# Performance work log

Measured on AMD Instinct MI355X. Metric: run time of the kernel, lower is better.

Reference implementation:

```python
import jax, jax.numpy as jnp
import numpy as np

B, LQ, LK, D = 16, 1024, 4096, 256
SQRT_SCALE_INV = 0.25          # D ** -0.25, so scale = 1/sqrt(D)
HALF_BW = 128 // 2             # stripe_bandwdith // 2
NEG_INF = float('-inf')


def setup_inputs() -> dict:
    key = jax.random.key(0)
    k1, k2, k3, k4 = jax.random.split(key, 4)
    query = jax.random.normal(k1, (B, LQ, D), jnp.float32)
    key_t = jax.random.normal(k2, (B, LK, D), jnp.float32)
    value = jax.random.normal(k3, (B, LK, D), jnp.float32)
    # key lengths in [LK//2, LK]; masked_fill in torch requires max == LK
    key_lengths = jax.random.randint(k4, (B,), LK // 2, LK + 1).astype(jnp.int32)
    key_lengths = key_lengths.at[0].set(LK)
    query_lengths = jnp.full((B,), LQ, dtype=jnp.int32)  # full so no all-masked rows
    mask = jnp.arange(LK)[None, :] < key_lengths[:, None]  # [B, LK] bool, True = valid
    return {"query": query, "key": key_t, "value": value, "mask": mask,
            "query_lengths": query_lengths, "key_lengths": key_lengths}


def _stripe_mask(query_lengths, key_lengths, Lq, Lk):
    # band around line y = x * (key_len / query_len), per sample
    gx = jnp.arange(Lq, dtype=jnp.float32)[None, :, None]   # [1,Lq,1]
    gy = jnp.arange(Lk, dtype=jnp.float32)[None, None, :]   # [1,1,Lk]
    slope = (key_lengths.astype(jnp.float32) /
             query_lengths.astype(jnp.float32))[:, None, None]  # [B,1,1]
    center = gx * slope
    return (gy >= center - HALF_BW) & (gy <= center + HALF_BW)  # [B,Lq,Lk] bool


def reference(query, key, value, mask, query_lengths, key_lengths):
    # scores = (q * s) @ (k * s)^T  ==  (q @ k^T) * s^2
    scores = jnp.einsum('bqd,bkd->bqk', query, key) * (SQRT_SCALE_INV * SQRT_SCALE_INV)
    stripe = _stripe_mask(query_lengths, key_lengths, query.shape[1], key.shape[1])
    full_mask = mask[:, None, :] & stripe                    # padding AND stripe
    scores = jnp.where(full_mask, scores.astype(jnp.float32), NEG_INF)
    weight = jax.nn.softmax(scores, axis=-1).astype(query.dtype)
    # module applies no dropout (p=0) and returns (attn_weight, value)
    return (weight, value)
```

## Files before the change

kernel.cpp:

```cpp
#include <hip/hip_runtime.h>
#include <math.h>

constexpr int B_  = 16;
constexpr int LQ_ = 1024;
constexpr int LK_ = 4096;
constexpr int D_  = 256;
constexpr float HALF_BW_F = 64.0f;
constexpr float SCALE = 0.0625f;

typedef float fx4 __attribute__((ext_vector_type(4)));

constexpr int NB_PAD = 168;
constexpr int ROWS_PER_BLK = 16;
constexpr int NBLK = (B_ * LQ_) / ROWS_PER_BLK;
constexpr int NXCD = 8;
constexpr int BLK_PER_XCD = NBLK / NXCD;

template <int CTRL>
__device__ __forceinline__ float dpp_add(float v) {
    int x = __builtin_amdgcn_update_dpp(0, __float_as_int(v), CTRL, 0xF, 0xF, true);
    return v + __int_as_float(x);
}

__device__ __forceinline__ float grp16_max(float v) {
    #pragma unroll
    for (int off = 8; off > 0; off >>= 1)
        v = fmaxf(v, __shfl_xor(v, off, 64));
    return v;
}
__device__ __forceinline__ float grp16_sum(float v) {
    #pragma unroll
    for (int off = 8; off > 0; off >>= 1)
        v += __shfl_xor(v, off, 64);
    return v;
}

__global__ __launch_bounds__(256, 4) void stripe_attn_kernel(
    const float* __restrict__ Q, const float* __restrict__ K,
    const float* __restrict__ V,
    const int* __restrict__ qlen, const int* __restrict__ klen,
    float* __restrict__ Wout, float* __restrict__ Vout)
{
    const int rb   = (blockIdx.x & (NXCD - 1)) * BLK_PER_XCD + (blockIdx.x >> 3);
    const int tid  = threadIdx.x;
    const int lane = tid & 63;
    const int wave = tid >> 6;
    const int g    = lane >> 4;
    const int l    = lane & 15;
    const int row0 = rb * ROWS_PER_BLK + wave * 4;
    const int b    = row0 >> 10;
    const int qi0  = row0 & (LQ_ - 1);

    __shared__ float s_sc[4][4 * NB_PAD];

    const int   key_len = klen[b];
    const float slope   = (float)key_len / (float)qlen[b];

    int k_lo[4], k_hi[4];
    #pragma unroll
    for (int r = 0; r < 4; ++r) {
        const float center = (float)(qi0 + r) * slope;
        int lo = (int)ceilf(center - HALF_BW_F); if (lo < 0) lo = 0;
        int hi = (int)floorf(center + HALF_BW_F); if (hi > key_len - 1) hi = key_len - 1;
        k_lo[r] = lo; k_hi[r] = hi;
    }
    const int lo0 = k_lo[0], hi3 = k_hi[3];

    {
        const fx4 z4 = {0.f, 0.f, 0.f, 0.f};
        #pragma unroll
        for (int r = 0; r < 4; ++r) {
            const int s_lo = k_lo[r] >> 8, s_hi = k_hi[r] >> 8;
            float* base = Wout + (size_t)(row0 + r) * LK_;
            #pragma unroll
            for (int j = 0; j < 16; ++j) {
                if (j < s_lo || j > s_hi)
                    __builtin_nontemporal_store(z4, (fx4*)(base + (j * 64 + lane) * 4));
            }
        }
    }

    {
        const float* vs = V    + (size_t)row0 * 1024;
        float*       vd = Vout + (size_t)row0 * 1024;
        #pragma unroll
        for (int it = 0; it < 16; ++it) {
            const int o = (it * 64 + lane) * 4;
            fx4 t = __builtin_nontemporal_load((const fx4*)(vs + o));
            __builtin_nontemporal_store(t, (fx4*)(vd + o));
        }
    }

    const float* qbase = Q + ((size_t)b * LQ_ + qi0) * D_;
    float4 q0[4], q1[4], q2[4], q3[4];
    #pragma unroll
    for (int m = 0; m < 4; ++m) {
        q0[m] = *(const float4*)(qbase + 0 * D_ + l * 16 + m * 4);
        q1[m] = *(const float4*)(qbase + 1 * D_ + l * 16 + m * 4);
        q2[m] = *(const float4*)(qbase + 2 * D_ + l * 16 + m * 4);
        q3[m] = *(const float4*)(qbase + 3 * D_ + l * 16 + m * 4);
    }

    const float* kbase = K + (size_t)b * LK_ * D_;
    float* sw = s_sc[wave];
    for (int kk0 = lo0; kk0 <= hi3; kk0 += 4) {
        const int key  = kk0 + g;
        const int keyc = (key <= hi3) ? key : hi3;
        const float* kp = kbase + (size_t)keyc * D_ + l * 16;
        float4 kf[4];
        #pragma unroll
        for (int m = 0; m < 4; ++m)
            kf[m] = *(const float4*)(kp + m * 4);
        float a0 = 0.f, a1 = 0.f, a2 = 0.f, a3 = 0.f;
        #pragma unroll
        for (int m = 0; m < 4; ++m) {
            a0 += q0[m].x*kf[m].x + q0[m].y*kf[m].y + q0[m].z*kf[m].z + q0[m].w*kf[m].w;
            a1 += q1[m].x*kf[m].x + q1[m].y*kf[m].y + q1[m].z*kf[m].z + q1[m].w*kf[m].w;
            a2 += q2[m].x*kf[m].x + q2[m].y*kf[m].y + q2[m].z*kf[m].z + q2[m].w*kf[m].w;
            a3 += q3[m].x*kf[m].x + q3[m].y*kf[m].y + q3[m].z*kf[m].z + q3[m].w*kf[m].w;
        }
        a0 = dpp_add<0x118>(a0); a0 = dpp_add<0x114>(a0);
        a0 = dpp_add<0x112>(a0); a0 = dpp_add<0x111>(a0);
        a1 = dpp_add<0x118>(a1); a1 = dpp_add<0x114>(a1);
        a1 = dpp_add<0x112>(a1); a1 = dpp_add<0x111>(a1);
        a2 = dpp_add<0x118>(a2); a2 = dpp_add<0x114>(a2);
        a2 = dpp_add<0x112>(a2); a2 = dpp_add<0x111>(a2);
        a3 = dpp_add<0x118>(a3); a3 = dpp_add<0x114>(a3);
        a3 = dpp_add<0x112>(a3); a3 = dpp_add<0x111>(a3);
        if (l == 15) {
            if (key >= k_lo[0] && key <= k_hi[0]) sw[0*NB_PAD + key - k_lo[0]] = a0 * SCALE;
            if (key >= k_lo[1] && key <= k_hi[1]) sw[1*NB_PAD + key - k_lo[1]] = a1 * SCALE;
            if (key >= k_lo[2] && key <= k_hi[2]) sw[2*NB_PAD + key - k_lo[2]] = a2 * SCALE;
            if (key >= k_lo[3] && key <= k_hi[3]) sw[3*NB_PAD + key - k_lo[3]] = a3 * SCALE;
        }
    }

    const float center_g = (float)(qi0 + g) * slope;
    int klo_g = (int)ceilf(center_g - HALF_BW_F); if (klo_g < 0) klo_g = 0;
    int khi_g = (int)floorf(center_g + HALF_BW_F); if (khi_g > key_len - 1) khi_g = key_len - 1;
    const int nb_g = khi_g - klo_g + 1;
    float* sg = sw + g * NB_PAD;

    float vj[9];
    #pragma unroll
    for (int j = 0; j < 9; ++j) {
        const int idx = l + j * 16;
        vj[j] = (idx < nb_g) ? sg[idx] : -INFINITY;
    }
    float mx = vj[0];
    #pragma unroll
    for (int j = 1; j < 9; ++j) mx = fmaxf(mx, vj[j]);
    mx = grp16_max(mx);

    float ej[9], ssum = 0.f;
    #pragma unroll
    for (int j = 0; j < 9; ++j) { ej[j] = __expf(vj[j] - mx); ssum += ej[j]; }
    ssum = grp16_sum(ssum);
    const float inv = 1.0f / ssum;
    #pragma unroll
    for (int j = 0; j < 9; ++j)
        sg[l + j * 16] = ej[j] * inv;

    #pragma unroll
    for (int r = 0; r < 4; ++r) {
        const int klo = k_lo[r], khi = k_hi[r];
        const int s_lo = klo >> 8, s_hi = khi >> 8;
        float* base = Wout + (size_t)(row0 + r) * LK_;
        const float* sr = sw + r * NB_PAD;
        for (int j = s_lo; j <= s_hi; ++j) {
            const int c0 = (j * 64 + lane) * 4;
            float w[4] = {0.f, 0.f, 0.f, 0.f};
            if (c0 + 3 >= klo && c0 <= khi) {
                #pragma unroll
                for (int i = 0; i < 4; ++i) {
                    const int c = c0 + i;
                    if (c >= klo && c <= khi) w[i] = sr[c - klo];
                }
            }
            fx4 w4; w4.x = w[0]; w4.y = w[1]; w4.z = w[2]; w4.w = w[3];
            __builtin_nontemporal_store(w4, (fx4*)(base + c0));
        }
    }
}

extern "C" void kernel_launch(void* const* d_in, const int* in_sizes, int n_in,
                              void* d_out, int out_size, void* d_ws, size_t ws_size,
                              hipStream_t stream) {
    const float* Q    = (const float*)d_in[0];
    const float* K    = (const float*)d_in[1];
    const float* V    = (const float*)d_in[2];
    const int*   qlen = (const int*)d_in[4];
    const int*   klen = (const int*)d_in[5];

    float* Wout = (float*)d_out;
    const size_t W_ELEMS = (size_t)B_ * LQ_ * LK_;
    float* Vout = Wout + W_ELEMS;

    stripe_attn_kernel<<<dim3(NBLK), dim3(256), 0, stream>>>(
        Q, K, V, qlen, klen, Wout, Vout);
}
```

Measured before the change: 114.7 us.

## Split zero-fill of off-band weights into a separate kernel; move V copy last

The zero stores for weight segments outside the stripe band now live in a second fill kernel launched after the compute kernel, instead of at the start of the single fused kernel. The value copy moves to the end of the compute kernel. The aim is to shorten the compute kernel so its band work is not delayed behind large streaming stores. In exchange it adds a second launch, and the two kernels run back to back on the same stream, so their stores can no longer overlap with compute.

```diff
diff --git a/kernel.cpp b/kernel.cpp
--- a/kernel.cpp
+++ b/kernel.cpp
@@ -12,9 +12,9 @@
 
 constexpr int NB_PAD = 168;
 constexpr int ROWS_PER_BLK = 16;
-constexpr int NBLK = (B_ * LQ_) / ROWS_PER_BLK;
+constexpr int NUNIT = (B_ * LQ_) / ROWS_PER_BLK;
 constexpr int NXCD = 8;
-constexpr int BLK_PER_XCD = NBLK / NXCD;
+constexpr int UNIT_PER_XCD = NUNIT / NXCD;
 
 template <int CTRL>
 __device__ __forceinline__ float dpp_add(float v) {
@@ -35,21 +35,23 @@
     return v;
 }
 
-__global__ __launch_bounds__(256, 4) void stripe_attn_kernel(
+
+__global__ __launch_bounds__(256, 4) void compute_kernel(
     const float* __restrict__ Q, const float* __restrict__ K,
     const float* __restrict__ V,
     const int* __restrict__ qlen, const int* __restrict__ klen,
     float* __restrict__ Wout, float* __restrict__ Vout)
 {
-    const int rb   = (blockIdx.x & (NXCD - 1)) * BLK_PER_XCD + (blockIdx.x >> 3);
+    const int Bid  = blockIdx.x;
+    const int rb   = (Bid & (NXCD - 1)) * UNIT_PER_XCD + (Bid >> 3);
     const int tid  = threadIdx.x;
     const int lane = tid & 63;
     const int wave = tid >> 6;
-    const int g    = lane >> 4;
-    const int l    = lane & 15;
     const int row0 = rb * ROWS_PER_BLK + wave * 4;
     const int b    = row0 >> 10;
     const int qi0  = row0 & (LQ_ - 1);
+    const int g    = lane >> 4;
+    const int l    = lane & 15;
 
     __shared__ float s_sc[4][4 * NB_PAD];
 
@@ -65,31 +67,6 @@
         k_lo[r] = lo; k_hi[r] = hi;
     }
     const int lo0 = k_lo[0], hi3 = k_hi[3];
-
-    {
-        const fx4 z4 = {0.f, 0.f, 0.f, 0.f};
-        #pragma unroll
-        for (int r = 0; r < 4; ++r) {
-            const int s_lo = k_lo[r] >> 8, s_hi = k_hi[r] >> 8;
-            float* base = Wout + (size_t)(row0 + r) * LK_;
-            #pragma unroll
-            for (int j = 0; j < 16; ++j) {
-                if (j < s_lo || j > s_hi)
-                    __builtin_nontemporal_store(z4, (fx4*)(base + (j * 64 + lane) * 4));
-            }
-        }
-    }
-
-    {
-        const float* vs = V    + (size_t)row0 * 1024;
-        float*       vd = Vout + (size_t)row0 * 1024;
-        #pragma unroll
-        for (int it = 0; it < 16; ++it) {
-            const int o = (it * 64 + lane) * 4;
-            fx4 t = __builtin_nontemporal_load((const fx4*)(vs + o));
-            __builtin_nontemporal_store(t, (fx4*)(vd + o));
-        }
-    }
 
     const float* qbase = Q + ((size_t)b * LQ_ + qi0) * D_;
     float4 q0[4], q1[4], q2[4], q3[4];
@@ -181,6 +158,49 @@
             __builtin_nontemporal_store(w4, (fx4*)(base + c0));
         }
     }
+
+    {
+        const float* vs = V    + (size_t)row0 * 1024;
+        float*       vd = Vout + (size_t)row0 * 1024;
+        #pragma unroll
+        for (int it = 0; it < 16; ++it) {
+            const int o = (it * 64 + lane) * 4;
+            fx4 t = __builtin_nontemporal_load((const fx4*)(vs + o));
+            __builtin_nontemporal_store(t, (fx4*)(vd + o));
+        }
+    }
+}
+
+__global__ void fill_kernel(
+    const int* __restrict__ qlen, const int* __restrict__ klen,
+    float* __restrict__ Wout)
+{
+    const int Bid  = blockIdx.x;
+    const int rb   = (Bid & (NXCD - 1)) * UNIT_PER_XCD + (Bid >> 3);
+    const int tid  = threadIdx.x;
+    const int lane = tid & 63;
+    const int wave = tid >> 6;
+    const int row0 = rb * ROWS_PER_BLK + wave * 4;
+    const int b    = row0 >> 10;
+    const int qi0  = row0 & (LQ_ - 1);
+
+    const int   key_len = klen[b];
+    const float slope   = (float)key_len / (float)qlen[b];
+
+    const fx4 z4 = {0.f, 0.f, 0.f, 0.f};
+    #pragma unroll
+    for (int r = 0; r < 4; ++r) {
+        const float center = (float)(qi0 + r) * slope;
+        int lo = (int)ceilf(center - HALF_BW_F); if (lo < 0) lo = 0;
+        int hi = (int)floorf(center + HALF_BW_F); if (hi > key_len - 1) hi = key_len - 1;
+        const int s_lo = lo >> 8, s_hi = hi >> 8;
+        float* base = Wout + (size_t)(row0 + r) * LK_;
+        #pragma unroll
+        for (int j = 0; j < 16; ++j) {
+            if (j < s_lo || j > s_hi)
+                __builtin_nontemporal_store(z4, (fx4*)(base + (j * 64 + lane) * 4));
+        }
+    }
 }
 
 extern "C" void kernel_launch(void* const* d_in, const int* in_sizes, int n_in,
@@ -196,6 +216,7 @@
     const size_t W_ELEMS = (size_t)B_ * LQ_ * LK_;
     float* Vout = Wout + W_ELEMS;
 
-    stripe_attn_kernel<<<dim3(NBLK), dim3(256), 0, stream>>>(
+    compute_kernel<<<dim3(NUNIT), dim3(256), 0, stream>>>(
         Q, K, V, qlen, klen, Wout, Vout);
-}
+    fill_kernel<<<dim3(NUNIT), dim3(256), 0, stream>>>(qlen, klen, Wout);
+}
```

New measurement: 132.8 us. +15.7%, slower.
